# Performance work log

Hardware: AMD Instinct MI355X
Metric: run time of the kernel (lower is better)

## Reference

```python
import jax, jax.numpy as jnp
import numpy as np

UNITS, ORDER, THETA, DT = 512, 256, 784.0, 1.0


def _lmu_AB(order, theta, dt):
    # Continuous-time Legendre delay system (Voelker & Eliasmith 2018)
    Q = np.arange(order, dtype=np.float64)
    R = (2.0 * Q + 1.0)[:, None] / theta
    i, j = np.meshgrid(Q, Q, indexing='ij')
    A = np.where(i < j, -1.0, (-1.0) ** (i - j + 1)) * R
    B = ((-1.0) ** Q)[:, None] * R
    # ZOH discretization: Ad = expm(A*dt); Bd = A^{-1}(Ad - I)B
    Ad = np.asarray(jax.scipy.linalg.expm(jnp.asarray(A * dt, dtype=jnp.float64)))
    Bd = np.linalg.solve(A, (Ad - np.eye(order)) @ B)
    # cell stores AT = (Ad - I)^T so that m <- m + m@AT + u@BT
    return (Ad - np.eye(order)).T.astype(np.float32), Bd.T.astype(np.float32)


def setup_inputs() -> dict:
    key = jax.random.key(0)
    ks = jax.random.split(key, 6)
    D = 1
    x = jax.random.normal(ks[0], (64, 1024, D), dtype=jnp.float32)
    # lecun_uniform: U(-sqrt(3/fan_in), sqrt(3/fan_in))
    ie = jax.random.uniform(ks[1], (D, 1), minval=-np.sqrt(3.0 / D), maxval=np.sqrt(3.0 / D), dtype=jnp.float32)
    he = jax.random.uniform(ks[2], (UNITS, 1), minval=-np.sqrt(3.0 / UNITS), maxval=np.sqrt(3.0 / UNITS), dtype=jnp.float32)
    me = jnp.zeros((ORDER, 1), dtype=jnp.float32)  # Constant(0) initializer
    # glorot_normal: std = sqrt(2/(fan_in+fan_out))
    ik = jax.random.normal(ks[3], (D, UNITS), dtype=jnp.float32) * np.sqrt(2.0 / (D + UNITS))
    hk = jax.random.normal(ks[4], (UNITS, UNITS), dtype=jnp.float32) * np.sqrt(2.0 / (2 * UNITS))
    mk = jax.random.normal(ks[5], (ORDER, UNITS), dtype=jnp.float32) * np.sqrt(2.0 / (ORDER + UNITS))
    AT, BT = _lmu_AB(ORDER, THETA / DT, DT)
    return {"x": x, "input_encoders": ie, "hidden_encoders": he, "memory_encoders": me,
            "input_kernel": ik, "hidden_kernel": hk, "memory_kernel": mk,
            "AT": jnp.asarray(AT), "BT": jnp.asarray(BT)}


def reference(x, input_encoders, hidden_encoders, memory_encoders,
              input_kernel, hidden_kernel, memory_kernel, AT, BT):
    B = x.shape[0]
    h0 = jnp.zeros((B, UNITS), dtype=x.dtype)
    m0 = jnp.zeros((B, ORDER), dtype=x.dtype)

    def step(carry, xt):  # xt: [B, D]
        h, m = carry
        u = xt @ input_encoders + h @ hidden_encoders + m @ memory_encoders  # [B,1]
        m = m + m @ AT + u @ BT                                             # [B,order]
        h = jnp.tanh(xt @ input_kernel + h @ hidden_kernel + m @ memory_kernel)
        return (h, m), h

    xs = jnp.transpose(x, (1, 0, 2))  # [T,B,D]
    _, hs = jax.lax.scan(step, (h0, m0), xs)
    return jnp.transpose(hs, (1, 0, 2))  # [B,T,units]
```

## Files before the change

kernel.cpp:

```cpp
#include <hip/hip_runtime.h>
#include <hip/hip_fp16.h>

typedef unsigned int u32;
typedef unsigned short u16;
typedef _Float16 half2v __attribute__((ext_vector_type(2)));

#define N_UNITS 512
#define N_ORDER 256
#define N_T     1024
#define N_B     64
#define KWG     4
#define PKT_STRIDE 288

__device__ inline float dot2f(u32 a, u32 b, float acc) {
    return __builtin_amdgcn_fdot2(__builtin_bit_cast(half2v, a),
                                  __builtin_bit_cast(half2v, b), acc, false);
}
__device__ inline u16 f2h_bits(float v) {
    _Float16 f = (_Float16)v;
    return __builtin_bit_cast(u16, f);
}
__device__ inline float hbits2f(u32 dw) {
    u16 s = (u16)(dw & 0xFFFFu);
    _Float16 f = __builtin_bit_cast(_Float16, s);
    return (float)f;
}
__device__ inline u32 pack_h2(float a, float b) {
    return (u32)f2h_bits(a) | ((u32)f2h_bits(b) << 16);
}
__device__ inline u32 aload(const u32* p) {
    return __hip_atomic_load(p, __ATOMIC_RELAXED, __HIP_MEMORY_SCOPE_AGENT);
}
__device__ inline void astore(u32* p, u32 v) {
    __hip_atomic_store(p, v, __ATOMIC_RELAXED, __HIP_MEMORY_SCOPE_AGENT);
}

__global__ __launch_bounds__(256)
void prep_hk(const float* __restrict__ hk, u32* __restrict__ hk2) {
    int tid = blockIdx.x * 256 + threadIdx.x;
    int kk = tid >> 9, c = tid & 511;
    hk2[tid] = pack_h2(hk[(2 * kk) * 512 + c], hk[(2 * kk + 1) * 512 + c]);
}

__global__ __launch_bounds__(512)
void prep_amk(const float* __restrict__ mk, const float* __restrict__ at,
              const float* __restrict__ bt,
              u32* __restrict__ amk2, float* __restrict__ bmk) {
    int bj = blockIdx.x, c = threadIdx.x;
    if (bj < 128) {
        int j0 = 2 * bj, j1 = j0 + 1;
        float a0 = mk[j0 * 512 + c];
        float a1 = mk[j1 * 512 + c];
        #pragma unroll 8
        for (int k = 0; k < 256; ++k) {
            float w = mk[k * 512 + c];
            a0 = fmaf(at[j0 * 256 + k], w, a0);
            a1 = fmaf(at[j1 * 256 + k], w, a1);
        }
        amk2[bj * 512 + c] = pack_h2(a0, a1);
    } else {
        float s = 0.f;
        #pragma unroll 8
        for (int k = 0; k < 256; ++k) s = fmaf(bt[k], mk[k * 512 + c], s);
        bmk[c] = s;
    }
}

__global__ __launch_bounds__(512, 2)
void lmu_main(const float* __restrict__ x, const float* __restrict__ ie,
              const float* __restrict__ he, const float* __restrict__ me,
              const float* __restrict__ ik, const float* __restrict__ bt,
              const float* __restrict__ at,
              const u32* __restrict__ hk2, const u32* __restrict__ amk2,
              const float* __restrict__ bmk,
              u32* __restrict__ pkt, float* __restrict__ out) {
    __shared__ float xs[N_T];
    __shared__ float he_sl[128], ik_sl[128], bmk_sl[128];
    __shared__ float me_sl[64], bt_sl[64];
    __shared__ __align__(16) u16 h_h16[N_UNITS];
    __shared__ __align__(16) u16 m_hi16[N_ORDER], m_lo16[N_ORDER];
    __shared__ __align__(16) float mf[N_ORDER];
    __shared__ __align__(16) float zbuf[512], ampart[512];
    __shared__ float upart[4];
    __shared__ float upw_s[3];

    const int tid  = threadIdx.x;
    const int g    = blockIdx.x;
    const int b    = g & 63;
    const int q    = g >> 6;
    const int kg   = tid >> 7;
    const int cl   = tid & 127;
    const int kg8  = tid >> 6;
    const int jl   = tid & 63;
    const int J    = 64 * q + jl;
    const int lane = tid & 63;

    for (int i = tid; i < N_T; i += 512) xs[i] = x[b * N_T + i];
    if (tid < 128) {
        he_sl[tid]  = he[128 * q + tid];
        ik_sl[tid]  = ik[128 * q + tid];
        bmk_sl[tid] = bmk[128 * q + tid];
    }
    if (tid < 64) { me_sl[tid] = me[J]; bt_sl[tid] = bt[J]; }
    h_h16[tid] = 0;
    if (tid < 256) { m_hi16[tid] = 0; m_lo16[tid] = 0; mf[tid] = 0.f; }
    if (tid < 4) upart[tid] = 0.f;
    if (tid < 3) upw_s[tid] = 0.f;
    const float ie0 = ie[0];

    u32 hk_w[64];
    #pragma unroll
    for (int i = 0; i < 64; ++i)
        hk_w[i] = hk2[(size_t)(64 * kg + i) * 512 + 128 * q + cl];
    u32 amk_w[32];
    #pragma unroll
    for (int i = 0; i < 32; ++i)
        amk_w[i] = amk2[(size_t)(32 * kg + i) * 512 + 128 * q + cl];
    float at_w[32];
    #pragma unroll
    for (int i = 0; i < 32; ++i)
        at_w[i] = at[(size_t)(32 * kg8 + i) * 256 + J];

    __syncthreads();

    const uint4*  h4  = reinterpret_cast<const uint4*>(h_h16)  + 16 * kg;
    const uint4*  mh4 = reinterpret_cast<const uint4*>(m_hi16) + 8 * kg;
    const uint4*  ml4 = reinterpret_cast<const uint4*>(m_lo16) + 8 * kg;
    const float4* mf4 = reinterpret_cast<const float4*>(mf)    + 8 * kg8;
    float* outb = out + (size_t)b * N_T * N_UNITS;

    for (int t = 0; t < N_T; ++t) {
        if (t > 0) {
            const u32 ep  = (u32)t;
            const int par = (t - 1) & 1;
            if (tid < 195) {
                int pi = (tid < 192) ? (tid >> 6) : (tid - 192);
                int q2 = pi + (pi >= q ? 1 : 0);
                const u32* base = pkt + (size_t)(par * 256 + b * 4 + q2) * PKT_STRIDE;
                if (tid < 192) {
                    int i = tid & 63;
                    u32 d0, d1, d2, d3;
                    for (;;) {
                        d0 = aload(base + 4 * i + 0);
                        d1 = aload(base + 4 * i + 1);
                        d2 = aload(base + 4 * i + 2);
                        d3 = aload(base + 4 * i + 3);
                        if (((((d0 >> 16) ^ ep) | ((d1 >> 16) ^ ep)) |
                             (((d2 >> 16) ^ ep) | ((d3 >> 16) ^ ep))) == 0) break;
                    }
                    if (i < 32) {
                        int idx = 64 * q2 + 2 * i;
                        float2 v;
                        v.x = hbits2f(d0) + hbits2f(d1);
                        v.y = hbits2f(d2) + hbits2f(d3);
                        *reinterpret_cast<float2*>(mf + idx) = v;
                        reinterpret_cast<u32*>(m_hi16)[idx >> 1] = (d0 & 0xFFFFu) | (d2 << 16);
                        reinterpret_cast<u32*>(m_lo16)[idx >> 1] = (d1 & 0xFFFFu) | (d3 << 16);
                    } else {
                        int i0 = (128 * q2 + 4 * i - 128) >> 1;
                        u32* hhp = reinterpret_cast<u32*>(h_h16);
                        hhp[i0 + 0] = (d0 & 0xFFFFu) | (d1 << 16);
                        hhp[i0 + 1] = (d2 & 0xFFFFu) | (d3 << 16);
                    }
                } else {
                    const u32* p6 = base + 256;
                    u32 d0, d1, d2, d3, d4, d5;
                    for (;;) {
                        d0 = aload(p6 + 0); d1 = aload(p6 + 1); d2 = aload(p6 + 2);
                        d3 = aload(p6 + 3); d4 = aload(p6 + 4); d5 = aload(p6 + 5);
                        u32 bad = ((((d0 >> 16) ^ ep) | ((d1 >> 16) ^ ep)) |
                                   (((d2 >> 16) ^ ep) | ((d3 >> 16) ^ ep))) |
                                  (((d4 >> 16) ^ ep) | ((d5 >> 16) ^ ep));
                        if (bad == 0) break;
                    }
                    upart[q2] = (hbits2f(d0) + hbits2f(d1)) + (hbits2f(d2) + hbits2f(d3))
                              + (hbits2f(d4) + hbits2f(d5));
                }
            }
        }
        __syncthreads();

        {
            float z0 = 0.f, z1 = 0.f, z2 = 0.f, z3 = 0.f;
            #pragma unroll
            for (int j = 0; j < 16; ++j) {
                uint4 h = h4[j];
                z0 = dot2f(h.x, hk_w[4 * j + 0], z0);
                z1 = dot2f(h.y, hk_w[4 * j + 1], z1);
                z2 = dot2f(h.z, hk_w[4 * j + 2], z2);
                z3 = dot2f(h.w, hk_w[4 * j + 3], z3);
            }
            #pragma unroll
            for (int j = 0; j < 8; ++j) {
                uint4 mh = mh4[j];
                uint4 ml = ml4[j];
                z0 = dot2f(mh.x, amk_w[4 * j + 0], z0); z0 = dot2f(ml.x, amk_w[4 * j + 0], z0);
                z1 = dot2f(mh.y, amk_w[4 * j + 1], z1); z1 = dot2f(ml.y, amk_w[4 * j + 1], z1);
                z2 = dot2f(mh.z, amk_w[4 * j + 2], z2); z2 = dot2f(ml.z, amk_w[4 * j + 2], z2);
                z3 = dot2f(mh.w, amk_w[4 * j + 3], z3); z3 = dot2f(ml.w, amk_w[4 * j + 3], z3);
            }
            zbuf[tid] = (z0 + z1) + (z2 + z3);
            float a0 = 0.f, a1 = 0.f, a2 = 0.f, a3 = 0.f;
            #pragma unroll
            for (int j = 0; j < 8; ++j) {
                float4 m4 = mf4[j];
                a0 = fmaf(m4.x, at_w[4 * j + 0], a0);
                a1 = fmaf(m4.y, at_w[4 * j + 1], a1);
                a2 = fmaf(m4.z, at_w[4 * j + 2], a2);
                a3 = fmaf(m4.w, at_w[4 * j + 3], a3);
            }
            ampart[tid] = (a0 + a1) + (a2 + a3);
        }
        __syncthreads();

        const bool pub = (t < N_T - 1);
        const u32 eph  = (u32)(t + 1) << 16;
        u32* myb = pkt + (size_t)((t & 1) * 256 + b * 4 + q) * PKT_STRIDE;
        float u = 0.f, hnew = 0.f, mnew = 0.f;
        if (tid < 192) {
            u = ((upart[0] + upart[1]) + (upart[2] + upart[3]))
              + ((upw_s[0] + upw_s[1]) + upw_s[2]) + xs[t] * ie0;
        }
        if (tid < 128) {
            float zf = (zbuf[tid] + zbuf[tid + 128]) + (zbuf[tid + 256] + zbuf[tid + 384])
                     + xs[t] * ik_sl[tid] + u * bmk_sl[tid];
            hnew = tanhf(zf);
            u16 hb = f2h_bits(hnew);
            if (pub) astore(myb + 128 + tid, (u32)hb | eph);
            outb[(size_t)t * N_UNITS + 128 * q + tid] = hnew;
            h_h16[128 * q + tid] = hb;
        } else if (tid < 192) {
            mnew = mf[J] + u * bt_sl[jl];
            #pragma unroll
            for (int gi = 0; gi < 8; ++gi) mnew += ampart[jl + 64 * gi];
            _Float16 hi = (_Float16)mnew;
            float lo = mnew - (float)hi;
            u16 mhi_b = __builtin_bit_cast(u16, hi);
            u16 mlo_b = f2h_bits(lo);
            if (pub) {
                astore(myb + 2 * jl,     (u32)mhi_b | eph);
                astore(myb + 2 * jl + 1, (u32)mlo_b | eph);
            }
            mf[J] = mnew;
            m_hi16[J] = mhi_b;
            m_lo16[J] = mlo_b;
        }

        float up_red = 0.f;
        if (pub && tid < 192) {
            float up = (tid < 128) ? hnew * he_sl[tid] : mnew * me_sl[tid - 128];
            #pragma unroll
            for (int off = 32; off > 0; off >>= 1) up += __shfl_down(up, off);
            if (lane == 0) {
                const int w = tid >> 6;
                _Float16 hi = (_Float16)up;
                float lo = up - (float)hi;
                astore(myb + 256 + 2 * w,     (u32)__builtin_bit_cast(u16, hi) | eph);
                astore(myb + 256 + 2 * w + 1, (u32)f2h_bits(lo) | eph);
                up_red = up;
            }
        }
        __syncthreads();
        if (pub && lane == 0 && tid < 192) upw_s[tid >> 6] = up_red;
    }
}

extern "C" void kernel_launch(void* const* d_in, const int* in_sizes, int n_in,
                              void* d_out, int out_size, void* d_ws, size_t ws_size,
                              hipStream_t stream) {
    const float* x  = (const float*)d_in[0];
    const float* ie = (const float*)d_in[1];
    const float* he = (const float*)d_in[2];
    const float* me = (const float*)d_in[3];
    const float* ik = (const float*)d_in[4];
    const float* hk = (const float*)d_in[5];
    const float* mk = (const float*)d_in[6];
    const float* at = (const float*)d_in[7];
    const float* bt = (const float*)d_in[8];

    u32*   hk2  = (u32*)d_ws;
    u32*   amk2 = hk2 + 256 * 512;
    float* bmk  = (float*)(amk2 + 128 * 512);
    u32*   pkt  = (u32*)(bmk + 512);

    prep_hk<<<512, 256, 0, stream>>>(hk, hk2);
    prep_amk<<<129, 512, 0, stream>>>(mk, at, bt, amk2, bmk);
    lmu_main<<<N_B * KWG, 512, 0, stream>>>(x, ie, he, me, ik, bt, at,
                                            hk2, amk2, bmk, pkt, (float*)d_out);
}
```

Before: 3.211 ms.

## Remap thread work to wave-local shuffle reductions and double-buffer shared state

Reassigns the per-thread work so each output column's partial dot products are held by adjacent lanes and reduced with cross-lane shuffles, instead of going through shared zbuf/ampart arrays. This removes two of the three block-wide barriers per timestep. The h and m state plus the u partials are double-buffered in padded shared arrays, so next-step writes do not race with current-step reads. All 8 waves now compute u partials, and the packet polling is split across more threads, which changes the peer-exchange layout and adds redundant lane computation.

```diff
diff --git a/kernel.cpp b/kernel.cpp
--- a/kernel.cpp
+++ b/kernel.cpp
@@ -77,23 +77,24 @@
     __shared__ float xs[N_T];
     __shared__ float he_sl[128], ik_sl[128], bmk_sl[128];
     __shared__ float me_sl[64], bt_sl[64];
-    __shared__ __align__(16) u16 h_h16[N_UNITS];
-    __shared__ __align__(16) u16 m_hi16[N_ORDER], m_lo16[N_ORDER];
-    __shared__ __align__(16) float mf[N_ORDER];
-    __shared__ __align__(16) float zbuf[512], ampart[512];
-    __shared__ float upart[4];
-    __shared__ float upw_s[3];
-
-    const int tid  = threadIdx.x;
-    const int g    = blockIdx.x;
-    const int b    = g & 63;
-    const int q    = g >> 6;
-    const int kg   = tid >> 7;
-    const int cl   = tid & 127;
-    const int kg8  = tid >> 6;
-    const int jl   = tid & 63;
-    const int J    = 64 * q + jl;
-    const int lane = tid & 63;
+    __shared__ __align__(16) u32   hst[2][288];
+    __shared__ __align__(16) u32   mhst[2][160], mlst[2][160];
+    __shared__ __align__(16) float mfst[2][288];
+    __shared__ __align__(16) float uvals[2][16];
+
+    const int tid = threadIdx.x;
+    const int g = blockIdx.x, b = g & 63, q = g >> 6;
+    const int w = tid >> 6, l = tid & 63;
+    const int kk  = l & 3;
+    const int cl  = 16 * w + (l >> 2);
+    const int C   = 128 * q + cl;
+    const int k8  = l & 7;
+    const int jl2 = 8 * w + (l >> 3);
+    const int J   = 64 * q + jl2;
+
+    const int HW16 = 144 * q + cl;
+    const int MW16 = 80 * q + jl2;
+    const int MFW  = 36 * (2 * q + (jl2 >> 5)) + (jl2 & 31);
 
     for (int i = tid; i < N_T; i += 512) xs[i] = x[b * N_T + i];
     if (tid < 128) {
@@ -101,167 +102,176 @@
         ik_sl[tid]  = ik[128 * q + tid];
         bmk_sl[tid] = bmk[128 * q + tid];
     }
-    if (tid < 64) { me_sl[tid] = me[J]; bt_sl[tid] = bt[J]; }
-    h_h16[tid] = 0;
-    if (tid < 256) { m_hi16[tid] = 0; m_lo16[tid] = 0; mf[tid] = 0.f; }
-    if (tid < 4) upart[tid] = 0.f;
-    if (tid < 3) upw_s[tid] = 0.f;
+    if (tid < 64) { me_sl[tid] = me[64 * q + tid]; bt_sl[tid] = bt[64 * q + tid]; }
+    for (int i = tid; i < 2 * 288; i += 512) {
+        (&hst[0][0])[i] = 0u;
+        (&mfst[0][0])[i] = 0.f;
+    }
+    for (int i = tid; i < 2 * 160; i += 512) {
+        (&mhst[0][0])[i] = 0u;
+        (&mlst[0][0])[i] = 0u;
+    }
+    if (tid < 32) (&uvals[0][0])[tid] = 0.f;
     const float ie0 = ie[0];
 
     u32 hk_w[64];
     #pragma unroll
     for (int i = 0; i < 64; ++i)
-        hk_w[i] = hk2[(size_t)(64 * kg + i) * 512 + 128 * q + cl];
+        hk_w[i] = hk2[(size_t)(64 * kk + i) * 512 + C];
     u32 amk_w[32];
     #pragma unroll
     for (int i = 0; i < 32; ++i)
-        amk_w[i] = amk2[(size_t)(32 * kg + i) * 512 + 128 * q + cl];
+        amk_w[i] = amk2[(size_t)(32 * kk + i) * 512 + C];
     float at_w[32];
     #pragma unroll
     for (int i = 0; i < 32; ++i)
-        at_w[i] = at[(size_t)(32 * kg8 + i) * 256 + J];
+        at_w[i] = at[(size_t)(32 * k8 + i) * 256 + J];
 
     __syncthreads();
 
-    const uint4*  h4  = reinterpret_cast<const uint4*>(h_h16)  + 16 * kg;
-    const uint4*  mh4 = reinterpret_cast<const uint4*>(m_hi16) + 8 * kg;
-    const uint4*  ml4 = reinterpret_cast<const uint4*>(m_lo16) + 8 * kg;
-    const float4* mf4 = reinterpret_cast<const float4*>(mf)    + 8 * kg8;
     float* outb = out + (size_t)b * N_T * N_UNITS;
 
     for (int t = 0; t < N_T; ++t) {
-        if (t > 0) {
+        const int sb = t & 1;
+
+        if (t > 0 && tid < 198) {
             const u32 ep  = (u32)t;
             const int par = (t - 1) & 1;
-            if (tid < 195) {
-                int pi = (tid < 192) ? (tid >> 6) : (tid - 192);
-                int q2 = pi + (pi >= q ? 1 : 0);
+            if (tid < 192) {
+                const int pi = tid >> 6;
+                const int q2 = pi + (pi >= q ? 1 : 0);
                 const u32* base = pkt + (size_t)(par * 256 + b * 4 + q2) * PKT_STRIDE;
-                if (tid < 192) {
-                    int i = tid & 63;
-                    u32 d0, d1, d2, d3;
-                    for (;;) {
-                        d0 = aload(base + 4 * i + 0);
-                        d1 = aload(base + 4 * i + 1);
-                        d2 = aload(base + 4 * i + 2);
-                        d3 = aload(base + 4 * i + 3);
-                        if (((((d0 >> 16) ^ ep) | ((d1 >> 16) ^ ep)) |
-                             (((d2 >> 16) ^ ep) | ((d3 >> 16) ^ ep))) == 0) break;
-                    }
-                    if (i < 32) {
-                        int idx = 64 * q2 + 2 * i;
-                        float2 v;
-                        v.x = hbits2f(d0) + hbits2f(d1);
-                        v.y = hbits2f(d2) + hbits2f(d3);
-                        *reinterpret_cast<float2*>(mf + idx) = v;
-                        reinterpret_cast<u32*>(m_hi16)[idx >> 1] = (d0 & 0xFFFFu) | (d2 << 16);
-                        reinterpret_cast<u32*>(m_lo16)[idx >> 1] = (d1 & 0xFFFFu) | (d3 << 16);
-                    } else {
-                        int i0 = (128 * q2 + 4 * i - 128) >> 1;
-                        u32* hhp = reinterpret_cast<u32*>(h_h16);
-                        hhp[i0 + 0] = (d0 & 0xFFFFu) | (d1 << 16);
-                        hhp[i0 + 1] = (d2 & 0xFFFFu) | (d3 << 16);
-                    }
+                const int i = tid & 63;
+                u32 d0, d1, d2, d3;
+                for (;;) {
+                    d0 = aload(base + 4 * i + 0);
+                    d1 = aload(base + 4 * i + 1);
+                    d2 = aload(base + 4 * i + 2);
+                    d3 = aload(base + 4 * i + 3);
+                    if (((((d0 >> 16) ^ ep) | ((d1 >> 16) ^ ep)) |
+                         (((d2 >> 16) ^ ep) | ((d3 >> 16) ^ ep))) == 0) break;
+                }
+                if (i < 32) {
+                    mhst[sb][40 * q2 + i] = (d0 & 0xFFFFu) | (d2 << 16);
+                    mlst[sb][40 * q2 + i] = (d1 & 0xFFFFu) | (d3 << 16);
+                    float2 v;
+                    v.x = hbits2f(d0) + hbits2f(d1);
+                    v.y = hbits2f(d2) + hbits2f(d3);
+                    *reinterpret_cast<float2*>(
+                        &mfst[sb][36 * (2 * q2 + (i >> 4)) + ((2 * i) & 31)]) = v;
                 } else {
-                    const u32* p6 = base + 256;
-                    u32 d0, d1, d2, d3, d4, d5;
-                    for (;;) {
-                        d0 = aload(p6 + 0); d1 = aload(p6 + 1); d2 = aload(p6 + 2);
-                        d3 = aload(p6 + 3); d4 = aload(p6 + 4); d5 = aload(p6 + 5);
-                        u32 bad = ((((d0 >> 16) ^ ep) | ((d1 >> 16) ^ ep)) |
-                                   (((d2 >> 16) ^ ep) | ((d3 >> 16) ^ ep))) |
-                                  (((d4 >> 16) ^ ep) | ((d5 >> 16) ^ ep));
-                        if (bad == 0) break;
-                    }
-                    upart[q2] = (hbits2f(d0) + hbits2f(d1)) + (hbits2f(d2) + hbits2f(d3))
-                              + (hbits2f(d4) + hbits2f(d5));
+                    const int dl = 2 * (i - 32);
+                    hst[sb][72 * q2 + dl]     = (d0 & 0xFFFFu) | (d1 << 16);
+                    hst[sb][72 * q2 + dl + 1] = (d2 & 0xFFFFu) | (d3 << 16);
                 }
+            } else {
+                const int ui = tid - 192;
+                const int pi = ui >> 1, half = ui & 1;
+                const int q2 = pi + (pi >= q ? 1 : 0);
+                const u32* p8 = pkt + (size_t)(par * 256 + b * 4 + q2) * PKT_STRIDE
+                              + 256 + 8 * half;
+                u32 d0, d1, d2, d3, d4, d5, d6, d7;
+                for (;;) {
+                    d0 = aload(p8 + 0); d1 = aload(p8 + 1);
+                    d2 = aload(p8 + 2); d3 = aload(p8 + 3);
+                    d4 = aload(p8 + 4); d5 = aload(p8 + 5);
+                    d6 = aload(p8 + 6); d7 = aload(p8 + 7);
+                    u32 bad = ((((d0 >> 16) ^ ep) | ((d1 >> 16) ^ ep)) |
+                               (((d2 >> 16) ^ ep) | ((d3 >> 16) ^ ep))) |
+                              ((((d4 >> 16) ^ ep) | ((d5 >> 16) ^ ep)) |
+                               (((d6 >> 16) ^ ep) | ((d7 >> 16) ^ ep)));
+                    if (bad == 0) break;
+                }
+                uvals[sb][2 * q2 + half] =
+                    ((hbits2f(d0) + hbits2f(d1)) + (hbits2f(d2) + hbits2f(d3)))
+                  + ((hbits2f(d4) + hbits2f(d5)) + (hbits2f(d6) + hbits2f(d7)));
             }
         }
         __syncthreads();
 
-        {
-            float z0 = 0.f, z1 = 0.f, z2 = 0.f, z3 = 0.f;
-            #pragma unroll
-            for (int j = 0; j < 16; ++j) {
-                uint4 h = h4[j];
-                z0 = dot2f(h.x, hk_w[4 * j + 0], z0);
-                z1 = dot2f(h.y, hk_w[4 * j + 1], z1);
-                z2 = dot2f(h.z, hk_w[4 * j + 2], z2);
-                z3 = dot2f(h.w, hk_w[4 * j + 3], z3);
-            }
-            #pragma unroll
-            for (int j = 0; j < 8; ++j) {
-                uint4 mh = mh4[j];
-                uint4 ml = ml4[j];
-                z0 = dot2f(mh.x, amk_w[4 * j + 0], z0); z0 = dot2f(ml.x, amk_w[4 * j + 0], z0);
-                z1 = dot2f(mh.y, amk_w[4 * j + 1], z1); z1 = dot2f(ml.y, amk_w[4 * j + 1], z1);
-                z2 = dot2f(mh.z, amk_w[4 * j + 2], z2); z2 = dot2f(ml.z, amk_w[4 * j + 2], z2);
-                z3 = dot2f(mh.w, amk_w[4 * j + 3], z3); z3 = dot2f(ml.w, amk_w[4 * j + 3], z3);
-            }
-            zbuf[tid] = (z0 + z1) + (z2 + z3);
-            float a0 = 0.f, a1 = 0.f, a2 = 0.f, a3 = 0.f;
-            #pragma unroll
-            for (int j = 0; j < 8; ++j) {
-                float4 m4 = mf4[j];
-                a0 = fmaf(m4.x, at_w[4 * j + 0], a0);
-                a1 = fmaf(m4.y, at_w[4 * j + 1], a1);
-                a2 = fmaf(m4.z, at_w[4 * j + 2], a2);
-                a3 = fmaf(m4.w, at_w[4 * j + 3], a3);
-            }
-            ampart[tid] = (a0 + a1) + (a2 + a3);
-        }
-        __syncthreads();
+        const uint4*  h4g  = reinterpret_cast<const uint4*>(&hst[sb][0])  + 18 * kk;
+        const uint4*  mh4g = reinterpret_cast<const uint4*>(&mhst[sb][0]) + 10 * kk;
+        const uint4*  ml4g = reinterpret_cast<const uint4*>(&mlst[sb][0]) + 10 * kk;
+        const float4* mf4g = reinterpret_cast<const float4*>(&mfst[sb][0]) + 9 * k8;
+
+        float z0 = 0.f, z1 = 0.f, z2 = 0.f, z3 = 0.f;
+        #pragma unroll
+        for (int j = 0; j < 16; ++j) {
+            uint4 hv = h4g[j];
+            z0 = dot2f(hv.x, hk_w[4 * j + 0], z0);
+            z1 = dot2f(hv.y, hk_w[4 * j + 1], z1);
+            z2 = dot2f(hv.z, hk_w[4 * j + 2], z2);
+            z3 = dot2f(hv.w, hk_w[4 * j + 3], z3);
+        }
+        #pragma unroll
+        for (int j = 0; j < 8; ++j) {
+            uint4 mh = mh4g[j], ml = ml4g[j];
+            z0 = dot2f(mh.x, amk_w[4 * j + 0], z0); z0 = dot2f(ml.x, amk_w[4 * j + 0], z0);
+            z1 = dot2f(mh.y, amk_w[4 * j + 1], z1); z1 = dot2f(ml.y, amk_w[4 * j + 1], z1);
+            z2 = dot2f(mh.z, amk_w[4 * j + 2], z2); z2 = dot2f(ml.z, amk_w[4 * j + 2], z2);
+            z3 = dot2f(mh.w, amk_w[4 * j + 3], z3); z3 = dot2f(ml.w, amk_w[4 * j + 3], z3);
+        }
+        float z = (z0 + z1) + (z2 + z3);
+        z += __shfl_xor(z, 1); z += __shfl_xor(z, 2);
+
+        float a0 = 0.f, a1 = 0.f, a2 = 0.f, a3 = 0.f;
+        #pragma unroll
+        for (int j = 0; j < 8; ++j) {
+            float4 mv = mf4g[j];
+            a0 = fmaf(mv.x, at_w[4 * j + 0], a0);
+            a1 = fmaf(mv.y, at_w[4 * j + 1], a1);
+            a2 = fmaf(mv.z, at_w[4 * j + 2], a2);
+            a3 = fmaf(mv.w, at_w[4 * j + 3], a3);
+        }
+        float am = (a0 + a1) + (a2 + a3);
+        am += __shfl_xor(am, 1); am += __shfl_xor(am, 2); am += __shfl_xor(am, 4);
+
+        const float4* uvp = reinterpret_cast<const float4*>(&uvals[sb][0]);
+        float4 ua = uvp[0], ub2 = uvp[1], uc = uvp[2], ud = uvp[3];
+        const float u = ((((ua.x + ua.y) + (ua.z + ua.w)) + ((ub2.x + ub2.y) + (ub2.z + ub2.w)))
+                      +  (((uc.x + uc.y) + (uc.z + uc.w)) + ((ud.x + ud.y) + (ud.z + ud.w))))
+                      + xs[t] * ie0;
 
         const bool pub = (t < N_T - 1);
         const u32 eph  = (u32)(t + 1) << 16;
-        u32* myb = pkt + (size_t)((t & 1) * 256 + b * 4 + q) * PKT_STRIDE;
-        float u = 0.f, hnew = 0.f, mnew = 0.f;
-        if (tid < 192) {
-            u = ((upart[0] + upart[1]) + (upart[2] + upart[3]))
-              + ((upw_s[0] + upw_s[1]) + upw_s[2]) + xs[t] * ie0;
-        }
-        if (tid < 128) {
-            float zf = (zbuf[tid] + zbuf[tid + 128]) + (zbuf[tid + 256] + zbuf[tid + 384])
-                     + xs[t] * ik_sl[tid] + u * bmk_sl[tid];
-            hnew = tanhf(zf);
-            u16 hb = f2h_bits(hnew);
-            if (pub) astore(myb + 128 + tid, (u32)hb | eph);
-            outb[(size_t)t * N_UNITS + 128 * q + tid] = hnew;
-            h_h16[128 * q + tid] = hb;
-        } else if (tid < 192) {
-            mnew = mf[J] + u * bt_sl[jl];
-            #pragma unroll
-            for (int gi = 0; gi < 8; ++gi) mnew += ampart[jl + 64 * gi];
-            _Float16 hi = (_Float16)mnew;
-            float lo = mnew - (float)hi;
-            u16 mhi_b = __builtin_bit_cast(u16, hi);
-            u16 mlo_b = f2h_bits(lo);
+        u32* myb = pkt + (size_t)(sb * 256 + b * 4 + q) * PKT_STRIDE;
+
+        const float mnew = mfst[sb][MFW] + u * bt_sl[jl2] + am;
+        const _Float16 mh_f = (_Float16)mnew;
+        const u16 mhi_b = __builtin_bit_cast(u16, mh_f);
+        const u16 mlo_b = f2h_bits(mnew - (float)mh_f);
+        if ((l & 7) == 0) {
             if (pub) {
-                astore(myb + 2 * jl,     (u32)mhi_b | eph);
-                astore(myb + 2 * jl + 1, (u32)mlo_b | eph);
+                astore(myb + 2 * jl2,     (u32)mhi_b | eph);
+                astore(myb + 2 * jl2 + 1, (u32)mlo_b | eph);
             }
-            mf[J] = mnew;
-            m_hi16[J] = mhi_b;
-            m_lo16[J] = mlo_b;
-        }
-
-        float up_red = 0.f;
-        if (pub && tid < 192) {
-            float up = (tid < 128) ? hnew * he_sl[tid] : mnew * me_sl[tid - 128];
-            #pragma unroll
-            for (int off = 32; off > 0; off >>= 1) up += __shfl_down(up, off);
-            if (lane == 0) {
-                const int w = tid >> 6;
-                _Float16 hi = (_Float16)up;
-                float lo = up - (float)hi;
+            reinterpret_cast<u16*>(&mhst[sb ^ 1][0])[MW16] = mhi_b;
+            reinterpret_cast<u16*>(&mlst[sb ^ 1][0])[MW16] = mlo_b;
+            mfst[sb ^ 1][MFW] = mnew;
+        }
+
+        const float zf = z + xs[t] * ik_sl[cl] + u * bmk_sl[cl];
+        const float hnew = tanhf(zf);
+        const u16 hb = f2h_bits(hnew);
+        if ((l & 3) == 0) {
+            if (pub) astore(myb + 128 + cl, (u32)hb | eph);
+            outb[(size_t)t * N_UNITS + C] = hnew;
+            reinterpret_cast<u16*>(&hst[sb ^ 1][0])[HW16] = hb;
+        }
+
+        if (pub) {
+            float up = ((l & 3) == 0) ? hnew * he_sl[cl] : 0.f;
+            if ((l & 7) == 0) up = fmaf(mnew, me_sl[jl2], up);
+            up += __shfl_xor(up, 1);  up += __shfl_xor(up, 2);
+            up += __shfl_xor(up, 4);  up += __shfl_xor(up, 8);
+            up += __shfl_xor(up, 16); up += __shfl_xor(up, 32);
+            if (l == 0) {
+                uvals[sb ^ 1][8 + w] = up;
+                const _Float16 hi = (_Float16)up;
                 astore(myb + 256 + 2 * w,     (u32)__builtin_bit_cast(u16, hi) | eph);
-                astore(myb + 256 + 2 * w + 1, (u32)f2h_bits(lo) | eph);
-                up_red = up;
+                astore(myb + 256 + 2 * w + 1, (u32)f2h_bits(up - (float)hi) | eph);
             }
         }
-        __syncthreads();
-        if (pub && lane == 0 && tid < 192) upw_s[tid >> 6] = up_red;
     }
 }
 
```

Measured after the change: 5.685 ms. +77.0%, slower.
